# Optimization experiments

Measured on AMD Instinct MI355X. Metric: run time of the kernel, lower is better.

Reference implementation:

```python
import jax, jax.numpy as jnp
import numpy as np

NCODEBOOKS, K, SUBVEC = 32, 16, 128
IN_F, OUT_F = 4096, 2048
BATCH, SEQ = 2, 1024


def setup_inputs() -> dict:
    key = jax.random.key(0)
    k1, k2, k3, k4, k5 = jax.random.split(key, 5)
    return {
        "x": jax.random.normal(k1, (BATCH, SEQ, IN_F), dtype=jnp.float32),
        "centroids": jax.random.normal(k2, (NCODEBOOKS, K, SUBVEC), dtype=jnp.float32),
        "weight": jax.random.normal(k3, (NCODEBOOKS, SUBVEC, OUT_F), dtype=jnp.float32),
        "inverse_temperature_logit": jax.random.normal(k4, (1,), dtype=jnp.float32),
        "bias": jax.random.normal(k5, (OUT_F,), dtype=jnp.float32),
    }


def reference(x, centroids, weight, inverse_temperature_logit, bias):
    shape = x.shape[:-1]
    C, k, d = centroids.shape
    # [N, C, d] -> [C, N, d]
    xr = jnp.transpose(x.reshape(-1, C, d), (1, 0, 2))
    # Euclidean cdist per codebook: [C, N, k]
    x2 = jnp.sum(xr * xr, axis=-1)[:, :, None]
    c2 = jnp.sum(centroids * centroids, axis=-1)[:, None, :]
    xc = jnp.einsum('cnd,ckd->cnk', xr, centroids)
    dist = jnp.sqrt(jnp.maximum(x2 + c2 - 2.0 * xc, 0.0))
    inv_temp = jax.nn.softplus(inverse_temperature_logit) + 1.0  # [1]
    attention = jax.nn.softmax(-dist * inv_temp, axis=-1)  # [C, N, k]
    lut = jnp.einsum('ckd,cdo->cko', centroids, weight)  # [C, k, O]
    training_output = jnp.einsum('cnk,cko->no', attention, lut)  # [N, O]
    # one-hot argmin matmul == direct gather of lut rows
    idx = jnp.argmin(dist, axis=-1)  # [C, N]
    gathered = jnp.take_along_axis(lut, idx[:, :, None], axis=1)  # [C, N, O]
    inference_output = jnp.sum(gathered, axis=0)  # [N, O]
    # straight-through estimator
    output = training_output - jax.lax.stop_gradient(training_output - inference_output)
    output = output + bias
    return output.reshape(*shape, lut.shape[-1])
```

## Files before the change

kernel.cpp:

```cpp
#include <hip/hip_runtime.h>

#define NCB 32
#define KK 16
#define DD 128
#define IN_F 4096
#define OUT_F 2048
#define NTOK 2048
#define LUT_BLOCKS 256
#define IDX_BLOCKS ((NTOK / 64) * NCB)

#define XS_STRIDE 148
#define CS_OFF (64 * XS_STRIDE)
#define SMEM_FLOATS (CS_OFF + KK * 164)

__global__ __launch_bounds__(256, 4) void fused_lut_idx(
    const float* __restrict__ centroids, const float* __restrict__ weight,
    const float* __restrict__ x, float* __restrict__ lut,
    unsigned char* __restrict__ idxb) {
    __shared__ float smem[SMEM_FLOATS];
    const int tid = threadIdx.x;

    if (blockIdx.x < LUT_BLOCKS) {
        const int c = blockIdx.x >> 3;
        const int o = ((blockIdx.x & 7) << 8) | tid;
        const float* cb = centroids + (size_t)c * KK * DD;
        const float* wb = weight + (size_t)c * DD * OUT_F + o;
        float acc[KK];
#pragma unroll
        for (int k = 0; k < KK; ++k) acc[k] = 0.f;
        for (int d4 = 0; d4 < DD / 4; ++d4) {
            float w0 = wb[(size_t)(d4 * 4 + 0) * OUT_F];
            float w1 = wb[(size_t)(d4 * 4 + 1) * OUT_F];
            float w2 = wb[(size_t)(d4 * 4 + 2) * OUT_F];
            float w3 = wb[(size_t)(d4 * 4 + 3) * OUT_F];
#pragma unroll
            for (int k = 0; k < KK; ++k) {
                float4 cv = *(const float4*)(cb + k * DD + d4 * 4);
                acc[k] += cv.x * w0 + cv.y * w1 + cv.z * w2 + cv.w * w3;
            }
        }
#pragma unroll
        for (int k = 0; k < KK; ++k)
            lut[((size_t)c * KK + k) * OUT_F + o] = acc[k];
    } else {
        const int bid = blockIdx.x - LUT_BLOCKS;
        const int c = bid & (NCB - 1);
        const int t0 = (bid >> 5) * 64;
        const int th_q = tid & 3;
        const int th_k = (tid >> 2) & 3;
        const int th_t = tid >> 4;
        float* xs = smem;
        float* cs = smem + CS_OFF;

        {
            const float* xg = x + (size_t)t0 * IN_F + c * DD;
#pragma unroll
            for (int i = 0; i < 8; ++i) {
                int p = i * 256 + tid;
                int t = p >> 5, f4 = p & 31;
                int q = f4 >> 3, jj = f4 & 7;
                float4 v = *(const float4*)(xg + (size_t)t * IN_F + f4 * 4);
                *(float4*)(xs + t * XS_STRIDE + q * 36 + jj * 4) = v;
            }
        }
        for (int p = tid; p < KK * 32; p += 256) {
            int k = p >> 5, f4 = p & 31;
            int q = f4 >> 3, jj = f4 & 7;
            *(float4*)(cs + k * 164 + q * 40 + jj * 4) =
                *(const float4*)(centroids + ((size_t)c * KK + k) * DD + f4 * 4);
        }
        __syncthreads();

        float acc[4][4], sq[4];
#pragma unroll
        for (int r = 0; r < 4; ++r)
#pragma unroll
            for (int kk = 0; kk < 4; ++kk) acc[r][kk] = 0.f;
#pragma unroll
        for (int kk = 0; kk < 4; ++kk) sq[kk] = 0.f;

#pragma unroll
        for (int chunk = 0; chunk < 8; ++chunk) {
            float4 ca[4];
#pragma unroll
            for (int kk = 0; kk < 4; ++kk)
                ca[kk] = *(const float4*)(cs + (th_k * 4 + kk) * 164 + th_q * 40 + chunk * 4);
#pragma unroll
            for (int kk = 0; kk < 4; ++kk)
                sq[kk] += ca[kk].x * ca[kk].x + ca[kk].y * ca[kk].y
                        + ca[kk].z * ca[kk].z + ca[kk].w * ca[kk].w;
#pragma unroll
            for (int r = 0; r < 4; ++r) {
                float4 xr = *(const float4*)(xs + (th_t * 4 + r) * XS_STRIDE
                                             + th_q * 36 + chunk * 4);
#pragma unroll
                for (int kk = 0; kk < 4; ++kk)
                    acc[r][kk] += xr.x * ca[kk].x + xr.y * ca[kk].y
                                + xr.z * ca[kk].z + xr.w * ca[kk].w;
            }
        }
#pragma unroll
        for (int kk = 0; kk < 4; ++kk) {
            float a = sq[kk];
            a += __shfl_xor(a, 1);
            a += __shfl_xor(a, 2);
            sq[kk] = a;
        }
#pragma unroll
        for (int r = 0; r < 4; ++r)
#pragma unroll
            for (int kk = 0; kk < 4; ++kk) {
                float a = acc[r][kk];
                a += __shfl_xor(a, 1);
                a += __shfl_xor(a, 2);
                acc[r][kk] = a;
            }
#pragma unroll
        for (int r = 0; r < 4; ++r) {
            float best = sq[0] - 2.f * acc[r][0];
            int bi = th_k * 4;
#pragma unroll
            for (int kk = 1; kk < 4; ++kk) {
                float v = sq[kk] - 2.f * acc[r][kk];
                if (v < best) { best = v; bi = th_k * 4 + kk; }
            }
#pragma unroll
            for (int s = 4; s <= 8; s <<= 1) {
                float ov = __shfl_xor(best, s);
                int oi = __shfl_xor(bi, s);
                if (ov < best || (ov == best && oi < bi)) { best = ov; bi = oi; }
            }
            if ((tid & 15) == 0)
                idxb[(size_t)(t0 + th_t * 4 + r) * NCB + c] = (unsigned char)bi;
        }
    }
}

__global__ __launch_bounds__(256) void gather_kernel(const float* __restrict__ lut,
                                                     const unsigned char* __restrict__ idxb,
                                                     const float* __restrict__ bias,
                                                     float* __restrict__ out) {
    const int t0 = blockIdx.x * 256;
    const int o0 = blockIdx.y * 32;
    __shared__ float slut[NCB * KK * 36];
    __shared__ unsigned char sidx[256 * NCB];

    {
        const int row = threadIdx.x >> 3;
        const int q = threadIdx.x & 7;
        for (int r = row; r < NCB * KK; r += 32)
            *(float4*)(slut + r * 36 + q * 4) =
                *(const float4*)(lut + (size_t)r * OUT_F + o0 + q * 4);
    }
    {
        const int4* ig = (const int4*)(idxb + (size_t)t0 * NCB);
        int4* is4 = (int4*)sidx;
        for (int i = threadIdx.x; i < 512; i += 256) is4[i] = ig[i];
    }
    __syncthreads();

    const int oo = (threadIdx.x & 7) * 4;
    const int tl = threadIdx.x >> 3;
    const float4 bv = *(const float4*)(bias + o0 + oo);

    for (int tt = tl; tt < 256; tt += 32) {
        float4 acc = bv;
        const unsigned int* ip = (const unsigned int*)(sidx + tt * NCB);
#pragma unroll
        for (int c4 = 0; c4 < NCB / 4; ++c4) {
            unsigned int iv4 = ip[c4];
#pragma unroll
            for (int b = 0; b < 4; ++b) {
                int cc = c4 * 4 + b;
                int iv = (iv4 >> (8 * b)) & 0xff;
                const float4 v = *(const float4*)(slut + (cc * KK + iv) * 36 + oo);
                acc.x += v.x; acc.y += v.y; acc.z += v.z; acc.w += v.w;
            }
        }
        *(float4*)(out + (size_t)(t0 + tt) * OUT_F + o0 + oo) = acc;
    }
}

extern "C" void kernel_launch(void* const* d_in, const int* in_sizes, int n_in,
                              void* d_out, int out_size, void* d_ws, size_t ws_size,
                              hipStream_t stream) {
    const float* x         = (const float*)d_in[0];
    const float* centroids = (const float*)d_in[1];
    const float* weight    = (const float*)d_in[2];
    const float* bias      = (const float*)d_in[4];
    float* out = (float*)d_out;

    float* lut = (float*)d_ws;
    unsigned char* idxb = (unsigned char*)d_ws + (4u << 20);

    fused_lut_idx<<<LUT_BLOCKS + IDX_BLOCKS, 256, 0, stream>>>(
        centroids, weight, x, lut, idxb);
    gather_kernel<<<dim3(NTOK / 256, OUT_F / 32), 256, 0, stream>>>(lut, idxb, bias, out);
}
```

Measured before the change: 149.6 us.

## Gather directly from global LUT, fold bias into LUT, retile LUT and idx blocks

The gather kernel no longer stages a 32-column LUT slice in shared memory. Each thread now reads LUT rows directly from global memory (relying on L2/cache), with an output-major grid and 128 tokens per block. The bias add moves into the codebook-0 LUT rows. The LUT blocks now compute float4 output columns for half the centroids each, and the index blocks process 32 tokens instead of 64 to give more blocks. The aim is to remove per-block LUT staging cost and raise parallelism, in exchange for uncoalesced random global gathers and more redundant loads of x-side data.

```diff
diff --git a/kernel.cpp b/kernel.cpp
--- a/kernel.cpp
+++ b/kernel.cpp
@@ -6,46 +6,62 @@
 #define IN_F 4096
 #define OUT_F 2048
 #define NTOK 2048
-#define LUT_BLOCKS 256
-#define IDX_BLOCKS ((NTOK / 64) * NCB)
+
+#define LUT_BLOCKS 128
+#define TT 32
+#define IDX_BLOCKS ((NTOK / TT) * NCB)
 
 #define XS_STRIDE 148
-#define CS_OFF (64 * XS_STRIDE)
+#define CS_OFF (TT * XS_STRIDE)
 #define SMEM_FLOATS (CS_OFF + KK * 164)
 
 __global__ __launch_bounds__(256, 4) void fused_lut_idx(
     const float* __restrict__ centroids, const float* __restrict__ weight,
-    const float* __restrict__ x, float* __restrict__ lut,
-    unsigned char* __restrict__ idxb) {
+    const float* __restrict__ x, const float* __restrict__ bias,
+    float* __restrict__ lut, unsigned char* __restrict__ idxb) {
     __shared__ float smem[SMEM_FLOATS];
     const int tid = threadIdx.x;
 
     if (blockIdx.x < LUT_BLOCKS) {
-        const int c = blockIdx.x >> 3;
-        const int o = ((blockIdx.x & 7) << 8) | tid;
-        const float* cb = centroids + (size_t)c * KK * DD;
+        const int c  = blockIdx.x >> 2;
+        const int kh = (blockIdx.x >> 1) & 1;
+        const int oh = blockIdx.x & 1;
+        const int o  = oh * 1024 + tid * 4;
+        const float* cb = centroids + ((size_t)c * KK + kh * 8) * DD;
         const float* wb = weight + (size_t)c * DD * OUT_F + o;
-        float acc[KK];
-#pragma unroll
-        for (int k = 0; k < KK; ++k) acc[k] = 0.f;
+        float4 acc[8];
+#pragma unroll
+        for (int k = 0; k < 8; ++k) acc[k] = make_float4(0.f, 0.f, 0.f, 0.f);
+#pragma unroll 2
         for (int d4 = 0; d4 < DD / 4; ++d4) {
-            float w0 = wb[(size_t)(d4 * 4 + 0) * OUT_F];
-            float w1 = wb[(size_t)(d4 * 4 + 1) * OUT_F];
-            float w2 = wb[(size_t)(d4 * 4 + 2) * OUT_F];
-            float w3 = wb[(size_t)(d4 * 4 + 3) * OUT_F];
-#pragma unroll
-            for (int k = 0; k < KK; ++k) {
+            float4 w0 = *(const float4*)(wb + (size_t)(d4 * 4 + 0) * OUT_F);
+            float4 w1 = *(const float4*)(wb + (size_t)(d4 * 4 + 1) * OUT_F);
+            float4 w2 = *(const float4*)(wb + (size_t)(d4 * 4 + 2) * OUT_F);
+            float4 w3 = *(const float4*)(wb + (size_t)(d4 * 4 + 3) * OUT_F);
+#pragma unroll
+            for (int k = 0; k < 8; ++k) {
                 float4 cv = *(const float4*)(cb + k * DD + d4 * 4);
-                acc[k] += cv.x * w0 + cv.y * w1 + cv.z * w2 + cv.w * w3;
-            }
-        }
-#pragma unroll
-        for (int k = 0; k < KK; ++k)
-            lut[((size_t)c * KK + k) * OUT_F + o] = acc[k];
+                acc[k].x += cv.x * w0.x + cv.y * w1.x + cv.z * w2.x + cv.w * w3.x;
+                acc[k].y += cv.x * w0.y + cv.y * w1.y + cv.z * w2.y + cv.w * w3.y;
+                acc[k].z += cv.x * w0.z + cv.y * w1.z + cv.z * w2.z + cv.w * w3.z;
+                acc[k].w += cv.x * w0.w + cv.y * w1.w + cv.z * w2.w + cv.w * w3.w;
+            }
+        }
+        if (c == 0) {
+            float4 bv = *(const float4*)(bias + o);
+#pragma unroll
+            for (int k = 0; k < 8; ++k) {
+                acc[k].x += bv.x; acc[k].y += bv.y;
+                acc[k].z += bv.z; acc[k].w += bv.w;
+            }
+        }
+#pragma unroll
+        for (int k = 0; k < 8; ++k)
+            *(float4*)(lut + ((size_t)c * KK + kh * 8 + k) * OUT_F + o) = acc[k];
     } else {
         const int bid = blockIdx.x - LUT_BLOCKS;
         const int c = bid & (NCB - 1);
-        const int t0 = (bid >> 5) * 64;
+        const int t0 = (bid >> 5) * TT;
         const int th_q = tid & 3;
         const int th_k = (tid >> 2) & 3;
         const int th_t = tid >> 4;
@@ -55,7 +71,7 @@
         {
             const float* xg = x + (size_t)t0 * IN_F + c * DD;
 #pragma unroll
-            for (int i = 0; i < 8; ++i) {
+            for (int i = 0; i < (TT * DD / 4) / 256; ++i) {
                 int p = i * 256 + tid;
                 int t = p >> 5, f4 = p & 31;
                 int q = f4 >> 3, jj = f4 & 7;
@@ -71,9 +87,9 @@
         }
         __syncthreads();
 
-        float acc[4][4], sq[4];
-#pragma unroll
-        for (int r = 0; r < 4; ++r)
+        float acc[2][4], sq[4];
+#pragma unroll
+        for (int r = 0; r < 2; ++r)
 #pragma unroll
             for (int kk = 0; kk < 4; ++kk) acc[r][kk] = 0.f;
 #pragma unroll
@@ -90,8 +106,8 @@
                 sq[kk] += ca[kk].x * ca[kk].x + ca[kk].y * ca[kk].y
                         + ca[kk].z * ca[kk].z + ca[kk].w * ca[kk].w;
 #pragma unroll
-            for (int r = 0; r < 4; ++r) {
-                float4 xr = *(const float4*)(xs + (th_t * 4 + r) * XS_STRIDE
+            for (int r = 0; r < 2; ++r) {
+                float4 xr = *(const float4*)(xs + (th_t * 2 + r) * XS_STRIDE
                                              + th_q * 36 + chunk * 4);
 #pragma unroll
                 for (int kk = 0; kk < 4; ++kk)
@@ -107,7 +123,7 @@
             sq[kk] = a;
         }
 #pragma unroll
-        for (int r = 0; r < 4; ++r)
+        for (int r = 0; r < 2; ++r)
 #pragma unroll
             for (int kk = 0; kk < 4; ++kk) {
                 float a = acc[r][kk];
@@ -116,7 +132,7 @@
                 acc[r][kk] = a;
             }
 #pragma unroll
-        for (int r = 0; r < 4; ++r) {
+        for (int r = 0; r < 2; ++r) {
             float best = sq[0] - 2.f * acc[r][0];
             int bi = th_k * 4;
 #pragma unroll
@@ -131,53 +147,39 @@
                 if (ov < best || (ov == best && oi < bi)) { best = ov; bi = oi; }
             }
             if ((tid & 15) == 0)
-                idxb[(size_t)(t0 + th_t * 4 + r) * NCB + c] = (unsigned char)bi;
+                idxb[(size_t)(t0 + th_t * 2 + r) * NCB + c] = (unsigned char)bi;
         }
     }
 }
 
 __global__ __launch_bounds__(256) void gather_kernel(const float* __restrict__ lut,
                                                      const unsigned char* __restrict__ idxb,
-                                                     const float* __restrict__ bias,
                                                      float* __restrict__ out) {
-    const int t0 = blockIdx.x * 256;
-    const int o0 = blockIdx.y * 32;
-    __shared__ float slut[NCB * KK * 36];
-    __shared__ unsigned char sidx[256 * NCB];
-
-    {
-        const int row = threadIdx.x >> 3;
-        const int q = threadIdx.x & 7;
-        for (int r = row; r < NCB * KK; r += 32)
-            *(float4*)(slut + r * 36 + q * 4) =
-                *(const float4*)(lut + (size_t)r * OUT_F + o0 + q * 4);
-    }
-    {
-        const int4* ig = (const int4*)(idxb + (size_t)t0 * NCB);
-        int4* is4 = (int4*)sidx;
-        for (int i = threadIdx.x; i < 512; i += 256) is4[i] = ig[i];
-    }
-    __syncthreads();
-
-    const int oo = (threadIdx.x & 7) * 4;
+    const int o0 = blockIdx.x * 32;
+    const int t0 = blockIdx.y * 128;
+    const int og = threadIdx.x & 7;
     const int tl = threadIdx.x >> 3;
-    const float4 bv = *(const float4*)(bias + o0 + oo);
-
-    for (int tt = tl; tt < 256; tt += 32) {
-        float4 acc = bv;
-        const unsigned int* ip = (const unsigned int*)(sidx + tt * NCB);
-#pragma unroll
-        for (int c4 = 0; c4 < NCB / 4; ++c4) {
-            unsigned int iv4 = ip[c4];
+    const int o = o0 + og * 4;
+
+#pragma unroll
+    for (int tt = 0; tt < 4; ++tt) {
+        const int t = t0 + tt * 32 + tl;
+        const uint4 iv0 = *(const uint4*)(idxb + (size_t)t * NCB);
+        const uint4 iv1 = *(const uint4*)(idxb + (size_t)t * NCB + 16);
+        unsigned int u[8] = {iv0.x, iv0.y, iv0.z, iv0.w, iv1.x, iv1.y, iv1.z, iv1.w};
+        float4 acc = make_float4(0.f, 0.f, 0.f, 0.f);
+#pragma unroll
+        for (int c4 = 0; c4 < 8; ++c4) {
+            unsigned int uv = u[c4];
 #pragma unroll
             for (int b = 0; b < 4; ++b) {
                 int cc = c4 * 4 + b;
-                int iv = (iv4 >> (8 * b)) & 0xff;
-                const float4 v = *(const float4*)(slut + (cc * KK + iv) * 36 + oo);
+                int k = (uv >> (8 * b)) & 0xff;
+                const float4 v = *(const float4*)(lut + (size_t)(cc * KK + k) * OUT_F + o);
                 acc.x += v.x; acc.y += v.y; acc.z += v.z; acc.w += v.w;
             }
         }
-        *(float4*)(out + (size_t)(t0 + tt) * OUT_F + o0 + oo) = acc;
+        *(float4*)(out + (size_t)t * OUT_F + o) = acc;
     }
 }
 
@@ -194,6 +196,6 @@
     unsigned char* idxb = (unsigned char*)d_ws + (4u << 20);
 
     fused_lut_idx<<<LUT_BLOCKS + IDX_BLOCKS, 256, 0, stream>>>(
-        centroids, weight, x, lut, idxb);
-    gather_kernel<<<dim3(NTOK / 256, OUT_F / 32), 256, 0, stream>>>(lut, idxb, bias, out);
+        centroids, weight, x, bias, lut, idxb);
+    gather_kernel<<<dim3(OUT_F / 32, NTOK / 128), 256, 0, stream>>>(lut, idxb, out);
 }
```

Measured after the change: 141.0 us. -5.7%, faster.
